# Performance work log

Measured on AMD Instinct MI355X. Metric: run time of the kernel, lower is better.

The kernel has to match this reference:

```python
import jax, jax.numpy as jnp
import numpy as np

B, N, D, H = 4, 2048, 1024, 16
HD = D // H


def setup_inputs() -> dict:
    key = jax.random.key(0)
    ks = jax.random.split(key, 9)
    s = 1.0 / np.sqrt(D)
    return {
        "x": jax.random.normal(ks[0], (B, N, D), jnp.float32),
        "Wq": jax.random.normal(ks[1], (D, D), jnp.float32) * s,
        "bq": jnp.zeros((D,), jnp.float32),
        "Wk": jax.random.normal(ks[2], (D, D), jnp.float32) * s,
        "bk": jnp.zeros((D,), jnp.float32),
        "Wv": jax.random.normal(ks[3], (D, D), jnp.float32) * s,
        "bv": jnp.zeros((D,), jnp.float32),
        "Wo": jax.random.normal(ks[4], (D, D), jnp.float32) * s,
        "bo": jnp.zeros((D,), jnp.float32),
    }


def reference(x, Wq, bq, Wk, bk, Wv, bv, Wo, bo):
    Bx, Nx, Dx = x.shape
    q = x @ Wq + bq  # [B,N,D]
    k = x @ Wk + bk
    v = x @ Wv + bv
    # split heads -> [B,H,N,hd]
    q = q.reshape(Bx, Nx, H, HD).transpose(0, 2, 1, 3)
    k = k.reshape(Bx, Nx, H, HD).transpose(0, 2, 1, 3)
    v = v.reshape(Bx, Nx, H, HD).transpose(0, 2, 1, 3)
    q = q / jnp.sqrt(jnp.asarray(HD, q.dtype))
    scores = jnp.einsum("bhqd,bhkd->bhqk", q, k)
    # causal mask: additive -1e9 strictly above diagonal (matches torch.triu diag=1)
    mask = jnp.triu(jnp.full((Nx, Nx), -1e9, dtype=scores.dtype), k=1)
    probs = jax.nn.softmax(scores + mask, axis=-1)
    out = jnp.einsum("bhqk,bhkd->bhqd", probs, v)  # [B,H,N,hd]
    out = out.transpose(0, 2, 1, 3).reshape(Bx, Nx, Dx)  # concat heads
    return out @ Wo + bo
```

## Files before the change

kernel.cpp:

```cpp
#include <hip/hip_runtime.h>
#include <hip/hip_bf16.h>


#define BB 4
#define NN 2048
#define DD 1024
#define HH 16
#define HD 64
#define MM (BB * NN)

typedef __bf16 bf16;
typedef __bf16 bf16x8 __attribute__((ext_vector_type(8)));
typedef float f32x4 __attribute__((ext_vector_type(4)));

__device__ __forceinline__ void async_copy16(bf16* lds, const bf16* g) {
    __builtin_amdgcn_global_load_lds(
        (const __attribute__((address_space(1))) void*)g,
        (__attribute__((address_space(3))) void*)lds, 16, 0, 0);
}

__global__ void convert_x(const float* __restrict__ x, bf16* __restrict__ xb) {
    int i = (blockIdx.x * 256 + threadIdx.x) * 4;
    float4 v = *(const float4*)&x[i];
    xb[i + 0] = (bf16)v.x;
    xb[i + 1] = (bf16)v.y;
    xb[i + 2] = (bf16)v.z;
    xb[i + 3] = (bf16)v.w;
}

__global__ void transpose_w(const float* __restrict__ W, bf16* __restrict__ Wt) {
    __shared__ float tile[32][33];
    int tx = threadIdx.x, ty = threadIdx.y;
    int x0 = blockIdx.x * 32, y0 = blockIdx.y * 32;
#pragma unroll
    for (int i = 0; i < 32; i += 8)
        tile[ty + i][tx] = W[(size_t)(y0 + ty + i) * DD + x0 + tx];
    __syncthreads();
#pragma unroll
    for (int i = 0; i < 32; i += 8)
        Wt[(size_t)(x0 + ty + i) * DD + y0 + tx] = (bf16)tile[tx][ty + i];
}

template <int MODE>
__global__ __launch_bounds__(256) void gemm_bt(
    const bf16* __restrict__ A, const bf16* __restrict__ Wt,
    const float* __restrict__ b0, const float* __restrict__ b1,
    const float* __restrict__ b2, void* __restrict__ out0,
    void* __restrict__ out1, void* __restrict__ out2) {
    const int K = DD;
    __shared__ __align__(16) bf16 As[128 * 32];
    __shared__ __align__(16) bf16 Bs[128 * 32];

    int m0 = blockIdx.x * 128;
    int n0 = blockIdx.y * 128;

    const bf16* Wz;
    const float* bias;
    void* out;
    float scale = 1.0f;
    int z = 0;
    if (MODE == 0) {
        z = blockIdx.z;
        Wz = Wt + (size_t)z * DD * DD;
        bias = (z == 0) ? b0 : ((z == 1) ? b1 : b2);
        out = (z == 0) ? out0 : ((z == 1) ? out1 : out2);
        if (z == 0) scale = 0.125f * 1.44269504f;
    } else {
        Wz = Wt; bias = b0; out = out0;
    }

    int tid = threadIdx.x;
    int w = tid >> 6, lane = tid & 63;
    int wm = w >> 1, wn = w & 1;
    int quad = lane >> 4, l16 = lane & 15;

    f32x4 acc[4][4];
#pragma unroll
    for (int i = 0; i < 4; i++)
#pragma unroll
        for (int j = 0; j < 4; j++) acc[i][j] = (f32x4){0.f, 0.f, 0.f, 0.f};

    for (int k0 = 0; k0 < K; k0 += 32) {
        __syncthreads();
#pragma unroll
        for (int j = 0; j < 2; j++) {
            int c = j * 256 + w * 64 + lane;
            int row = c >> 2, kk = (c & 3) * 8;
            async_copy16(&As[c * 8], &A[(size_t)(m0 + row) * K + k0 + kk]);
            async_copy16(&Bs[c * 8], &Wz[(size_t)(n0 + row) * K + k0 + kk]);
        }
        __syncthreads();

        bf16x8 af[4], bfm[4];
#pragma unroll
        for (int i = 0; i < 4; i++) {
            af[i] = *(const bf16x8*)&As[(wm * 64 + i * 16 + l16) * 32 + quad * 8];
            bfm[i] = *(const bf16x8*)&Bs[(wn * 64 + i * 16 + l16) * 32 + quad * 8];
        }
#pragma unroll
        for (int i = 0; i < 4; i++)
#pragma unroll
            for (int j = 0; j < 4; j++)
                acc[i][j] = __builtin_amdgcn_mfma_f32_16x16x32_bf16(
                    af[i], bfm[j], acc[i][j], 0, 0, 0);
    }

#pragma unroll
    for (int j = 0; j < 4; j++) {
        int n = n0 + wn * 64 + j * 16 + l16;
        float bv = bias[n];
#pragma unroll
        for (int i = 0; i < 4; i++) {
            int mrow = m0 + wm * 64 + i * 16 + quad * 4;
#pragma unroll
            for (int r = 0; r < 4; r++) {
                float v = (acc[i][j][r] + bv) * scale;
                int m = mrow + r;
                if (MODE == 0) {
                    int bidx = m >> 11;
                    int tok = m & (NN - 1);
                    int hh = n >> 6, hd = n & 63;
                    if (z == 2)
                        ((bf16*)out)[(((size_t)(bidx * HH + hh)) * HD + hd) * NN + tok] = (bf16)v;
                    else
                        ((bf16*)out)[(((size_t)(bidx * HH + hh)) * NN + tok) * HD + hd] = (bf16)v;
                } else {
                    ((float*)out)[(size_t)m * DD + n] = v;
                }
            }
        }
    }
}

__global__ __launch_bounds__(256) void flash_attn(
    const bf16* __restrict__ Q, const bf16* __restrict__ Kg,
    const bf16* __restrict__ Vt_g, bf16* __restrict__ Oc) {
    __shared__ __align__(16) bf16 Ks[128 * 72];
    __shared__ __align__(16) bf16 Vs[64 * 136];
    __shared__ __align__(16) bf16 Ps[128 * 136];

    int bh = blockIdx.y;
    int b = bh >> 4, h = bh & 15;
    int tid = threadIdx.x;
    int w = tid >> 6, lane = tid & 63;
    int quad = lane >> 4, l16 = lane & 15;

    const bf16* Qb = Q + (size_t)bh * NN * HD;
    const bf16* Kb = Kg + (size_t)bh * NN * HD;
    const bf16* Vtb = Vt_g + (size_t)bh * HD * NN;

    bf16x8 ones;
#pragma unroll
    for (int i = 0; i < 8; i++) ones[i] = (bf16)1.0f;

    for (int phase = 0; phase < 2; phase++) {
        int qi = (phase == 0) ? blockIdx.x : (15 - blockIdx.x);
        int q0 = qi * 128;

        bf16x8 qf[2][2];
#pragma unroll
        for (int mi = 0; mi < 2; mi++)
#pragma unroll
            for (int ks = 0; ks < 2; ks++)
                qf[mi][ks] = *(const bf16x8*)&Qb[(size_t)(q0 + w * 32 + mi * 16 + l16) * HD +
                                                ks * 32 + quad * 8];

        f32x4 l_sum[2];
        f32x4 o_acc[2][4];
#pragma unroll
        for (int mi = 0; mi < 2; mi++) {
            l_sum[mi] = (f32x4){0.f, 0.f, 0.f, 0.f};
#pragma unroll
            for (int di = 0; di < 4; di++) o_acc[mi][di] = (f32x4){0.f, 0.f, 0.f, 0.f};
        }

        int wave_qmax = q0 + w * 32 + 31;
        int kv_end = q0 + 128;

        for (int kv0 = 0; kv0 < kv_end; kv0 += 128) {
            __syncthreads();

#pragma unroll
            for (int j = 0; j < 4; j++) {
                int c = j * 256 + tid;
                int r = c >> 3, c8 = (c & 7) * 8;
                *(bf16x8*)&Ks[r * 72 + c8] = *(const bf16x8*)&Kb[(size_t)(kv0 + r) * HD + c8];
            }
#pragma unroll
            for (int j = 0; j < 4; j++) {
                int c = j * 256 + tid;
                int d = c >> 4, k8 = (c & 15) * 8;
                *(bf16x8*)&Vs[d * 136 + k8] = *(const bf16x8*)&Vtb[(size_t)d * NN + kv0 + k8];
            }
            __syncthreads();

            if (kv0 <= wave_qmax) {
#pragma unroll
                for (int ni = 0; ni < 8; ni++) {
                    bf16x8 bk0 = *(const bf16x8*)&Ks[(ni * 16 + l16) * 72 + quad * 8];
                    bf16x8 bk1 = *(const bf16x8*)&Ks[(ni * 16 + l16) * 72 + 32 + quad * 8];
                    f32x4 s0 = (f32x4){0.f, 0.f, 0.f, 0.f};
                    f32x4 s1 = (f32x4){0.f, 0.f, 0.f, 0.f};
                    s0 = __builtin_amdgcn_mfma_f32_16x16x32_bf16(qf[0][0], bk0, s0, 0, 0, 0);
                    s0 = __builtin_amdgcn_mfma_f32_16x16x32_bf16(qf[0][1], bk1, s0, 0, 0, 0);
                    s1 = __builtin_amdgcn_mfma_f32_16x16x32_bf16(qf[1][0], bk0, s1, 0, 0, 0);
                    s1 = __builtin_amdgcn_mfma_f32_16x16x32_bf16(qf[1][1], bk1, s1, 0, 0, 0);
                    int col = kv0 + ni * 16 + l16;
#pragma unroll
                    for (int r = 0; r < 4; r++) {
                        int row0 = q0 + w * 32 + quad * 4 + r;
                        float p0 = (col > row0) ? 0.f : exp2f(s0[r]);
                        float p1 = (col > row0 + 16) ? 0.f : exp2f(s1[r]);
                        Ps[(w * 32 + quad * 4 + r) * 136 + ni * 16 + l16] = (bf16)p0;
                        Ps[(w * 32 + 16 + quad * 4 + r) * 136 + ni * 16 + l16] = (bf16)p1;
                    }
                }

#pragma unroll
                for (int ks = 0; ks < 4; ks++) {
                    bf16x8 pf0 = *(const bf16x8*)&Ps[(w * 32 + l16) * 136 + ks * 32 + quad * 8];
                    bf16x8 pf1 = *(const bf16x8*)&Ps[(w * 32 + 16 + l16) * 136 + ks * 32 + quad * 8];
                    l_sum[0] = __builtin_amdgcn_mfma_f32_16x16x32_bf16(pf0, ones, l_sum[0], 0, 0, 0);
                    l_sum[1] = __builtin_amdgcn_mfma_f32_16x16x32_bf16(pf1, ones, l_sum[1], 0, 0, 0);
#pragma unroll
                    for (int di = 0; di < 4; di++) {
                        bf16x8 bv = *(const bf16x8*)&Vs[(di * 16 + l16) * 136 + ks * 32 + quad * 8];
                        o_acc[0][di] = __builtin_amdgcn_mfma_f32_16x16x32_bf16(pf0, bv, o_acc[0][di], 0, 0, 0);
                        o_acc[1][di] = __builtin_amdgcn_mfma_f32_16x16x32_bf16(pf1, bv, o_acc[1][di], 0, 0, 0);
                    }
                }
            }
        }

#pragma unroll
        for (int mi = 0; mi < 2; mi++)
#pragma unroll
            for (int r = 0; r < 4; r++) {
                float inv = 1.0f / l_sum[mi][r];
                int tok = q0 + w * 32 + mi * 16 + quad * 4 + r;
#pragma unroll
                for (int di = 0; di < 4; di++) {
                    int d = h * 64 + di * 16 + l16;
                    Oc[((size_t)(b * NN + tok)) * DD + d] = (bf16)(o_acc[mi][di][r] * inv);
                }
            }
    }
}

extern "C" void kernel_launch(void* const* d_in, const int* in_sizes, int n_in,
                              void* d_out, int out_size, void* d_ws, size_t ws_size,
                              hipStream_t stream) {
    const float* x  = (const float*)d_in[0];
    const float* Wq = (const float*)d_in[1];
    const float* bq = (const float*)d_in[2];
    const float* Wk = (const float*)d_in[3];
    const float* bk = (const float*)d_in[4];
    const float* Wv = (const float*)d_in[5];
    const float* bv = (const float*)d_in[6];
    const float* Wo = (const float*)d_in[7];
    const float* bo = (const float*)d_in[8];

    const size_t need = (size_t)(8388608ull * 5 + 4194304ull) * sizeof(bf16);
    if (ws_size < need) return;

    bf16* ws = (bf16*)d_ws;
    bf16* xb = ws;
    bf16* wt = xb + (size_t)MM * DD;
    bf16* Qw = wt + 4ull * DD * DD;
    bf16* Kw = Qw + (size_t)MM * DD;
    bf16* Vw = Kw + (size_t)MM * DD;
    bf16* Aw = Vw + (size_t)MM * DD;

    convert_x<<<dim3(MM * DD / 1024), 256, 0, stream>>>(x, xb);

    dim3 tb(32, 8);
    transpose_w<<<dim3(32, 32), tb, 0, stream>>>(Wq, wt + 0ull * DD * DD);
    transpose_w<<<dim3(32, 32), tb, 0, stream>>>(Wk, wt + 1ull * DD * DD);
    transpose_w<<<dim3(32, 32), tb, 0, stream>>>(Wv, wt + 2ull * DD * DD);
    transpose_w<<<dim3(32, 32), tb, 0, stream>>>(Wo, wt + 3ull * DD * DD);

    gemm_bt<0><<<dim3(MM / 128, DD / 128, 3), 256, 0, stream>>>(
        xb, wt, bq, bk, bv, Qw, Kw, Vw);

    flash_attn<<<dim3(8, BB * HH), 256, 0, stream>>>(Qw, Kw, Vw, Aw);

    gemm_bt<1><<<dim3(MM / 128, DD / 128, 1), 256, 0, stream>>>(
        Aw, wt + 3ull * DD * DD, bo, bo, bo, d_out, d_out, d_out);
}
```

Before: 293.8 us.

## Read K/V fragments directly from global memory and split masked diagonal tile

Removes the shared-memory staging of K and V tiles and the block-wide barriers around it; each wave now loads its MFMA operands straight from global memory (relying on L1/L2 for reuse across waves). The causal mask check is only applied on the diagonal tile via a template specialization, and exp2f is replaced with the hardware exp2 intrinsic. This trades LDS traffic and synchronization for redundant global/cache loads by all four waves. It also drops the per-wave skip of fully masked tiles on the diagonal, so every wave now processes the diagonal tile.

```diff
diff --git a/kernel.cpp b/kernel.cpp
--- a/kernel.cpp
+++ b/kernel.cpp
@@ -132,11 +132,56 @@
     }
 }
 
+template <bool MASKED>
+__device__ __forceinline__ void fa_tile(
+    const bf16* __restrict__ Kb, const bf16* __restrict__ Vtb, bf16* Ps,
+    const bf16x8 qf[2][2], f32x4 l_sum[2], f32x4 o_acc[2][4],
+    int kv0, int w, int quad, int l16, const bf16x8& ones) {
+#pragma unroll
+    for (int ni = 0; ni < 8; ni++) {
+        const bf16* kp = &Kb[(size_t)(kv0 + ni * 16 + l16) * HD + quad * 8];
+        bf16x8 bk0 = *(const bf16x8*)kp;
+        bf16x8 bk1 = *(const bf16x8*)(kp + 32);
+        f32x4 s0 = (f32x4){0.f, 0.f, 0.f, 0.f};
+        f32x4 s1 = (f32x4){0.f, 0.f, 0.f, 0.f};
+        s0 = __builtin_amdgcn_mfma_f32_16x16x32_bf16(qf[0][0], bk0, s0, 0, 0, 0);
+        s0 = __builtin_amdgcn_mfma_f32_16x16x32_bf16(qf[0][1], bk1, s0, 0, 0, 0);
+        s1 = __builtin_amdgcn_mfma_f32_16x16x32_bf16(qf[1][0], bk0, s1, 0, 0, 0);
+        s1 = __builtin_amdgcn_mfma_f32_16x16x32_bf16(qf[1][1], bk1, s1, 0, 0, 0);
+#pragma unroll
+        for (int r = 0; r < 4; r++) {
+            float p0, p1;
+            if (MASKED) {
+                int col = ni * 16 + l16;
+                int row0 = w * 32 + quad * 4 + r;
+                p0 = (col > row0) ? 0.f : __builtin_amdgcn_exp2f(s0[r]);
+                p1 = (col > row0 + 16) ? 0.f : __builtin_amdgcn_exp2f(s1[r]);
+            } else {
+                p0 = __builtin_amdgcn_exp2f(s0[r]);
+                p1 = __builtin_amdgcn_exp2f(s1[r]);
+            }
+            Ps[(w * 32 + quad * 4 + r) * 136 + ni * 16 + l16] = (bf16)p0;
+            Ps[(w * 32 + 16 + quad * 4 + r) * 136 + ni * 16 + l16] = (bf16)p1;
+        }
+    }
+#pragma unroll
+    for (int ks = 0; ks < 4; ks++) {
+        bf16x8 pf0 = *(const bf16x8*)&Ps[(w * 32 + l16) * 136 + ks * 32 + quad * 8];
+        bf16x8 pf1 = *(const bf16x8*)&Ps[(w * 32 + 16 + l16) * 136 + ks * 32 + quad * 8];
+        l_sum[0] = __builtin_amdgcn_mfma_f32_16x16x32_bf16(pf0, ones, l_sum[0], 0, 0, 0);
+        l_sum[1] = __builtin_amdgcn_mfma_f32_16x16x32_bf16(pf1, ones, l_sum[1], 0, 0, 0);
+#pragma unroll
+        for (int di = 0; di < 4; di++) {
+            bf16x8 bv = *(const bf16x8*)&Vtb[(size_t)(di * 16 + l16) * NN + kv0 + ks * 32 + quad * 8];
+            o_acc[0][di] = __builtin_amdgcn_mfma_f32_16x16x32_bf16(pf0, bv, o_acc[0][di], 0, 0, 0);
+            o_acc[1][di] = __builtin_amdgcn_mfma_f32_16x16x32_bf16(pf1, bv, o_acc[1][di], 0, 0, 0);
+        }
+    }
+}
+
 __global__ __launch_bounds__(256) void flash_attn(
     const bf16* __restrict__ Q, const bf16* __restrict__ Kg,
     const bf16* __restrict__ Vt_g, bf16* __restrict__ Oc) {
-    __shared__ __align__(16) bf16 Ks[128 * 72];
-    __shared__ __align__(16) bf16 Vs[64 * 136];
     __shared__ __align__(16) bf16 Ps[128 * 136];
 
     int bh = blockIdx.y;
@@ -174,63 +219,9 @@
             for (int di = 0; di < 4; di++) o_acc[mi][di] = (f32x4){0.f, 0.f, 0.f, 0.f};
         }
 
-        int wave_qmax = q0 + w * 32 + 31;
-        int kv_end = q0 + 128;
-
-        for (int kv0 = 0; kv0 < kv_end; kv0 += 128) {
-            __syncthreads();
-
-#pragma unroll
-            for (int j = 0; j < 4; j++) {
-                int c = j * 256 + tid;
-                int r = c >> 3, c8 = (c & 7) * 8;
-                *(bf16x8*)&Ks[r * 72 + c8] = *(const bf16x8*)&Kb[(size_t)(kv0 + r) * HD + c8];
-            }
-#pragma unroll
-            for (int j = 0; j < 4; j++) {
-                int c = j * 256 + tid;
-                int d = c >> 4, k8 = (c & 15) * 8;
-                *(bf16x8*)&Vs[d * 136 + k8] = *(const bf16x8*)&Vtb[(size_t)d * NN + kv0 + k8];
-            }
-            __syncthreads();
-
-            if (kv0 <= wave_qmax) {
-#pragma unroll
-                for (int ni = 0; ni < 8; ni++) {
-                    bf16x8 bk0 = *(const bf16x8*)&Ks[(ni * 16 + l16) * 72 + quad * 8];
-                    bf16x8 bk1 = *(const bf16x8*)&Ks[(ni * 16 + l16) * 72 + 32 + quad * 8];
-                    f32x4 s0 = (f32x4){0.f, 0.f, 0.f, 0.f};
-                    f32x4 s1 = (f32x4){0.f, 0.f, 0.f, 0.f};
-                    s0 = __builtin_amdgcn_mfma_f32_16x16x32_bf16(qf[0][0], bk0, s0, 0, 0, 0);
-                    s0 = __builtin_amdgcn_mfma_f32_16x16x32_bf16(qf[0][1], bk1, s0, 0, 0, 0);
-                    s1 = __builtin_amdgcn_mfma_f32_16x16x32_bf16(qf[1][0], bk0, s1, 0, 0, 0);
-                    s1 = __builtin_amdgcn_mfma_f32_16x16x32_bf16(qf[1][1], bk1, s1, 0, 0, 0);
-                    int col = kv0 + ni * 16 + l16;
-#pragma unroll
-                    for (int r = 0; r < 4; r++) {
-                        int row0 = q0 + w * 32 + quad * 4 + r;
-                        float p0 = (col > row0) ? 0.f : exp2f(s0[r]);
-                        float p1 = (col > row0 + 16) ? 0.f : exp2f(s1[r]);
-                        Ps[(w * 32 + quad * 4 + r) * 136 + ni * 16 + l16] = (bf16)p0;
-                        Ps[(w * 32 + 16 + quad * 4 + r) * 136 + ni * 16 + l16] = (bf16)p1;
-                    }
-                }
-
-#pragma unroll
-                for (int ks = 0; ks < 4; ks++) {
-                    bf16x8 pf0 = *(const bf16x8*)&Ps[(w * 32 + l16) * 136 + ks * 32 + quad * 8];
-                    bf16x8 pf1 = *(const bf16x8*)&Ps[(w * 32 + 16 + l16) * 136 + ks * 32 + quad * 8];
-                    l_sum[0] = __builtin_amdgcn_mfma_f32_16x16x32_bf16(pf0, ones, l_sum[0], 0, 0, 0);
-                    l_sum[1] = __builtin_amdgcn_mfma_f32_16x16x32_bf16(pf1, ones, l_sum[1], 0, 0, 0);
-#pragma unroll
-                    for (int di = 0; di < 4; di++) {
-                        bf16x8 bv = *(const bf16x8*)&Vs[(di * 16 + l16) * 136 + ks * 32 + quad * 8];
-                        o_acc[0][di] = __builtin_amdgcn_mfma_f32_16x16x32_bf16(pf0, bv, o_acc[0][di], 0, 0, 0);
-                        o_acc[1][di] = __builtin_amdgcn_mfma_f32_16x16x32_bf16(pf1, bv, o_acc[1][di], 0, 0, 0);
-                    }
-                }
-            }
-        }
+        for (int t = 0; t < qi; t++)
+            fa_tile<false>(Kb, Vtb, Ps, qf, l_sum, o_acc, t * 128, w, quad, l16, ones);
+        fa_tile<true>(Kb, Vtb, Ps, qf, l_sum, o_acc, q0, w, quad, l16, ones);
 
 #pragma unroll
         for (int mi = 0; mi < 2; mi++)
```

Result: slower. 363.0 us (+23.6%).
